# Optimization experiments

Measured on AMD Instinct MI355X. Metric: run time of the kernel, lower is better.

The kernel has to match this reference:

```python
import jax, jax.numpy as jnp
import numpy as np

B, T, NL, H, IN, OUT = 64, 25, 2, 2048, 66, 66
HT_LIMIT = 1.0  # hardtanh clamp


def setup_inputs() -> dict:
    key = jax.random.key(0)
    ks = jax.random.split(key, 14)
    s = 0.02  # small init like uniform(-1/sqrt(H), 1/sqrt(H))
    return {
        "inputs": jax.random.normal(ks[0], (B, IN), jnp.float32),
        "hiddens": jax.random.normal(ks[1], (NL, B, H), jnp.float32) * 0.1,
        "cells": jax.random.normal(ks[2], (NL, B, H), jnp.float32) * 0.1,
        "W_ih0": jax.random.normal(ks[3], (4 * H, IN), jnp.float32) * s,
        "W_hh0": jax.random.normal(ks[4], (4 * H, H), jnp.float32) * s,
        "b_ih0": jax.random.normal(ks[5], (4 * H,), jnp.float32) * s,
        "b_hh0": jax.random.normal(ks[6], (4 * H,), jnp.float32) * s,
        "W_ih1": jax.random.normal(ks[7], (4 * H, H), jnp.float32) * s,
        "W_hh1": jax.random.normal(ks[8], (4 * H, H), jnp.float32) * s,
        "b_ih1": jax.random.normal(ks[9], (4 * H,), jnp.float32) * s,
        "b_hh1": jax.random.normal(ks[10], (4 * H,), jnp.float32) * s,
        "fc_w": jax.random.normal(ks[11], (OUT, H), jnp.float32) * s,
        "fc_b": jax.random.normal(ks[12], (OUT,), jnp.float32) * s,
    }


def _lstm_cell(x, h, c, Wih, Whh, bih, bhh):
    # torch.nn.LSTMCell math: gates ordered i, f, g, o
    g = x @ Wih.T + bih + h @ Whh.T + bhh  # [B, 4H]
    i, f, gg, o = jnp.split(g, 4, axis=-1)
    i = jax.nn.sigmoid(i)
    f = jax.nn.sigmoid(f)
    gg = jnp.tanh(gg)
    o = jax.nn.sigmoid(o)
    c2 = f * c + i * gg
    h2 = o * jnp.tanh(c2)
    return h2, c2


def reference(inputs, hiddens, cells, W_ih0, W_hh0, b_ih0, b_hh0,
              W_ih1, W_hh1, b_ih1, b_hh1, fc_w, fc_b):
    params = [(W_ih0, W_hh0, b_ih0, b_hh0), (W_ih1, W_hh1, b_ih1, b_hh1)]
    # dropout p = 0.0 -> identity on inputs

    def step(carry, _):
        x, hs, cs = carry  # hs, cs: [NL, B, H]
        new_h, new_c = [], []
        layer_in = x
        for l, (Wih, Whh, bih, bhh) in enumerate(params):
            h2, c2 = _lstm_cell(layer_in, hs[l], cs[l], Wih, Whh, bih, bhh)
            new_h.append(h2)
            new_c.append(c2)
            layer_in = h2
        out = jnp.clip(new_h[-1] @ fc_w.T + fc_b, -HT_LIMIT, HT_LIMIT)  # hardtanh
        x_next = jax.lax.stop_gradient(out)  # output.detach() feedback
        return (x_next, jnp.stack(new_h), jnp.stack(new_c)), out

    _, outs = jax.lax.scan(step, (inputs, hiddens, cells), None, length=T)
    return jnp.transpose(outs, (1, 0, 2))  # [B, T, OUT]
```

## Files before the change

kernel.cpp:

```cpp
#include <hip/hip_runtime.h>
#include <hip/hip_bf16.h>


typedef short bfrag  __attribute__((ext_vector_type(8)));
typedef float accv   __attribute__((ext_vector_type(4)));
typedef float vfloat4 __attribute__((ext_vector_type(4)));
typedef unsigned short usvec8 __attribute__((ext_vector_type(8)));

#define LD8(p) (*(const bfrag*)(p))

__device__ __forceinline__ unsigned short f2bf(float x) {
    unsigned int u = __float_as_uint(x);
    unsigned int r = u + 0x7FFFu + ((u >> 16) & 1u);
    return (unsigned short)(r >> 16);
}
__device__ __forceinline__ float bf2f(unsigned short u) {
    return __uint_as_float(((unsigned int)u) << 16);
}

__device__ __forceinline__ int ap_idx(int b, int j, int KC) {
    return (((b >> 4) * KC + (j >> 5)) << 9) + ((((j >> 3) & 3) * 16 + (b & 15)) << 3) + (j & 7);
}


__global__ __launch_bounds__(256) void cast_big(
        const float* __restrict__ s0, const float* __restrict__ s1, const float* __restrict__ s2,
        unsigned short* __restrict__ d0, unsigned short* __restrict__ d1, unsigned short* __restrict__ d2) {
    unsigned int tid = blockIdx.x * 256 + threadIdx.x;
    unsigned int a = tid >> 21;
    unsigned int r = tid & 2097151u;
    const float* src = (a == 0) ? s0 : (a == 1) ? s1 : s2;
    unsigned short* dst = (a == 0) ? d0 : (a == 1) ? d1 : d2;
    unsigned int lane = r & 63u;
    unsigned int kc   = (r >> 6) & 63u;
    unsigned int p    = (r >> 12) & 1u;
    unsigned int jb   = r >> 13;
    unsigned int n = lane & 15u, quad = lane >> 4;
    unsigned int row = (2u * p + (n >> 3)) * 2048u + jb * 8u + (n & 7u);
    unsigned int k0  = kc * 32u + quad * 8u;
    const float* sp = src + (size_t)row * 2048 + k0;
    vfloat4 v0 = *(const vfloat4*)sp;
    vfloat4 v1 = *(const vfloat4*)(sp + 4);
    usvec8 u = { f2bf(v0.x), f2bf(v0.y), f2bf(v0.z), f2bf(v0.w),
                 f2bf(v1.x), f2bf(v1.y), f2bf(v1.z), f2bf(v1.w) };
    *(usvec8*)(dst + (size_t)r * 8) = u;
}

__global__ __launch_bounds__(256) void init_state(
        const float* __restrict__ inputs, const float* __restrict__ hiddens,
        const float* __restrict__ cells,  const float* __restrict__ wih0,
        unsigned short* __restrict__ wih0p,
        unsigned short* __restrict__ h0, unsigned short* __restrict__ h1,
        float* __restrict__ c0, float* __restrict__ c1,
        unsigned short* __restrict__ xb,
        float* __restrict__ bsum0, float* __restrict__ bsum1,
        const float* __restrict__ bih0, const float* __restrict__ bhh0,
        const float* __restrict__ bih1, const float* __restrict__ bhh1) {
    int i = blockIdx.x * 256 + threadIdx.x;
    if (i < 786432) {
        int jo = i & 7, lane = (i >> 3) & 63;
        int t2 = i >> 9, kc = t2 % 3, t3 = t2 / 3, p = t3 & 1, jb = t3 >> 1;
        int n = lane & 15, quad = lane >> 4;
        int row = (2 * p + (n >> 3)) * 2048 + jb * 8 + (n & 7);
        int k = kc * 32 + quad * 8 + jo;
        wih0p[i] = (k < 66) ? f2bf(wih0[row * 66 + k]) : (unsigned short)0;
        return;
    }
    i -= 786432;
    if (i < 131072) { int b = i >> 11, j = i & 2047; h0[ap_idx(b, j, 64)] = f2bf(hiddens[i]); return; }
    i -= 131072;
    if (i < 131072) { int b = i >> 11, j = i & 2047; h1[ap_idx(b, j, 64)] = f2bf(hiddens[131072 + i]); return; }
    i -= 131072;
    if (i < 131072) { int b = i >> 11, j = i & 2047; c0[(j >> 3) * 512 + b * 8 + (j & 7)] = cells[i]; return; }
    i -= 131072;
    if (i < 131072) { int b = i >> 11, j = i & 2047; c1[(j >> 3) * 512 + b * 8 + (j & 7)] = cells[131072 + i]; return; }
    i -= 131072;
    if (i < 16384) {
        int jo = i & 7, lane = (i >> 3) & 63;
        int t2 = i >> 9;
        int kc = t2 & 7, m = t2 >> 3;
        int b = m * 16 + (lane & 15);
        int k = kc * 32 + (lane >> 4) * 8 + jo;
        xb[i] = (k < 66) ? f2bf(inputs[b * 66 + k]) : (unsigned short)0;
        return;
    }
    i -= 16384;
    if (i < 8192) { bsum0[i] = bih0[i] + bhh0[i]; return; }
    i -= 8192;
    if (i < 8192) { bsum1[i] = bih1[i] + bhh1[i]; }
}

template<bool L0>
__global__ __launch_bounds__(512, 4) void lstm3(
        const unsigned short* __restrict__ Ap1, const unsigned short* __restrict__ Bp1,
        const unsigned short* __restrict__ Ap2, const unsigned short* __restrict__ Bp2,
        const float* __restrict__ bsum,
        float* __restrict__ c_state,
        unsigned short* __restrict__ h_out) {
    __shared__ float gsm[8][64][32];
    int tid = threadIdx.x, lane = tid & 63, w = tid >> 6;
    int jb = blockIdx.x;
    constexpr int N1  = L0 ? 1 : 8;
    constexpr int N2  = 8;
    constexpr int NC  = N1 + N2;
    constexpr int KA1 = L0 ? 8 : 64;
    constexpr int KB1 = L0 ? 3 : 64;
    constexpr int KC2 = 64;
    constexpr int PF  = 2;

    int kB1 = L0 ? (w < 3 ? w : 0) : w;
    const unsigned short* a1 = Ap1 + ((size_t)w << 9) + lane * 8;
    const unsigned short* b1 = Bp1 + (((size_t)(2 * jb) * KB1 + kB1) << 9) + lane * 8;
    const unsigned short* a2 = Ap2 + ((size_t)w << 9) + lane * 8;
    const unsigned short* b2 = Bp2 + (((size_t)(2 * jb) * KC2 + w) << 9) + lane * 8;

    accv acc[4][2] = {};
    bfrag fA[PF][4], fB[PF][2];

    auto issue = [&](int i) {
        int s = i % PF;
        const unsigned short *ap, *bp;
        int sa, sb;
        if (i < N1) { ap = a1 + ((size_t)i << 12); bp = b1 + ((size_t)i << 12); sa = KA1 << 9; sb = KB1 << 9; }
        else { int ii = i - N1; ap = a2 + ((size_t)ii << 12); bp = b2 + ((size_t)ii << 12); sa = KC2 << 9; sb = KC2 << 9; }
        fA[s][0] = LD8(ap);
        fA[s][1] = LD8(ap + sa);
        fA[s][2] = LD8(ap + 2 * sa);
        fA[s][3] = LD8(ap + 3 * sa);
        fB[s][0] = LD8(bp);
        fB[s][1] = LD8(bp + sb);
    };

    #pragma unroll
    for (int i = 0; i < PF; ++i) issue(i);
    #pragma unroll
    for (int i = 0; i < NC; ++i) {
        int s = i % PF;
        #pragma unroll
        for (int mi = 0; mi < 4; ++mi)
            #pragma unroll
            for (int p = 0; p < 2; ++p)
                acc[mi][p] = __builtin_amdgcn_mfma_f32_16x16x32_bf16(fA[s][mi], fB[s][p], acc[mi][p], 0, 0, 0);
        if (i + PF < NC) issue(i + PF);
    }

    int n = lane & 15, quad = lane >> 4;
    #pragma unroll
    for (int mi = 0; mi < 4; ++mi)
        #pragma unroll
        for (int p = 0; p < 2; ++p)
            #pragma unroll
            for (int r = 0; r < 4; ++r) {
                int R = mi * 16 + quad * 4 + r;
                int C = p * 16 + n;
                gsm[w][R][C ^ ((R & 3) << 3)] = acc[mi][p][r];
            }
    __syncthreads();

    int b = tid >> 3, jj = tid & 7;
    float g4[4];
    #pragma unroll
    for (int g = 0; g < 4; ++g) {
        int Cp = (g * 8 + jj) ^ ((b & 3) << 3);
        float s = 0.f;
        #pragma unroll
        for (int w8 = 0; w8 < 8; ++w8) s += gsm[w8][b][Cp];
        g4[g] = s;
    }
    int j = jb * 8 + jj;
    float gi = g4[0] + bsum[j];
    float gf = g4[1] + bsum[2048 + j];
    float gg = g4[2] + bsum[4096 + j];
    float go = g4[3] + bsum[6144 + j];
    float iv = 1.f / (1.f + __expf(-gi));
    float fv = 1.f / (1.f + __expf(-gf));
    float gv = tanhf(gg);
    float ov = 1.f / (1.f + __expf(-go));
    float cp = c_state[jb * 512 + tid];
    float cn = fv * cp + iv * gv;
    float hn = ov * tanhf(cn);
    c_state[jb * 512 + tid] = cn;
    h_out[ap_idx(b, j, 64)] = f2bf(hn);
}

__global__ __launch_bounds__(512) void fc2(
        const unsigned short* __restrict__ h1,
        const float* __restrict__ fcw,
        const float* __restrict__ fcb,
        float* __restrict__ out,
        unsigned short* __restrict__ xb,
        int t) {
    __shared__ float red[8][64];
    int o = blockIdx.x;
    int b = threadIdx.x & 63, w = threadIdx.x >> 6;
    const float* wrow = fcw + (size_t)o * 2048;
    float acc = 0.f;
    for (int kc = w; kc < 64; kc += 8) {
        const unsigned short* hp = h1 + (((size_t)(b >> 4) * 64 + kc) << 9) + (b & 15) * 8;
        const float* wp = wrow + kc * 32;
        #pragma unroll
        for (int q = 0; q < 4; ++q) {
            usvec8 hv = *(const usvec8*)(hp + q * 128);
            vfloat4 w0 = *(const vfloat4*)(wp + q * 8);
            vfloat4 w1 = *(const vfloat4*)(wp + q * 8 + 4);
            acc = fmaf(bf2f(hv[0]), w0.x, acc);
            acc = fmaf(bf2f(hv[1]), w0.y, acc);
            acc = fmaf(bf2f(hv[2]), w0.z, acc);
            acc = fmaf(bf2f(hv[3]), w0.w, acc);
            acc = fmaf(bf2f(hv[4]), w1.x, acc);
            acc = fmaf(bf2f(hv[5]), w1.y, acc);
            acc = fmaf(bf2f(hv[6]), w1.z, acc);
            acc = fmaf(bf2f(hv[7]), w1.w, acc);
        }
    }
    red[w][b] = acc;
    __syncthreads();
    if (threadIdx.x < 64) {
        int bb = threadIdx.x;
        float v = fcb[o];
        #pragma unroll
        for (int q = 0; q < 8; ++q) v += red[q][bb];
        v = fminf(1.f, fmaxf(-1.f, v));
        out[((size_t)bb * 25 + t) * 66 + o] = v;
        int kc = o >> 5;
        xb[(((size_t)(bb >> 4) * 8 + kc) << 9) + ((((o >> 3) & 3) * 16 + (bb & 15)) << 3) + (o & 7)] = f2bf(v);
    }
}

extern "C" void kernel_launch(void* const* d_in, const int* in_sizes, int n_in,
                              void* d_out, int out_size, void* d_ws, size_t ws_size,
                              hipStream_t stream) {
    (void)in_sizes; (void)n_in; (void)out_size; (void)ws_size;
    const float* inputs  = (const float*)d_in[0];
    const float* hiddens = (const float*)d_in[1];
    const float* cells   = (const float*)d_in[2];
    const float* W_ih0   = (const float*)d_in[3];
    const float* W_hh0   = (const float*)d_in[4];
    const float* b_ih0   = (const float*)d_in[5];
    const float* b_hh0   = (const float*)d_in[6];
    const float* W_ih1   = (const float*)d_in[7];
    const float* W_hh1   = (const float*)d_in[8];
    const float* b_ih1   = (const float*)d_in[9];
    const float* b_hh1   = (const float*)d_in[10];
    const float* fc_w    = (const float*)d_in[11];
    const float* fc_b    = (const float*)d_in[12];
    float* out = (float*)d_out;

    unsigned short* whh0p = (unsigned short*)d_ws;
    unsigned short* wih1p = whh0p + 16777216;
    unsigned short* whh1p = wih1p + 16777216;
    unsigned short* wih0p = whh1p + 16777216;
    unsigned short* h0a   = wih0p + 786432;
    unsigned short* h0b   = h0a + 131072;
    unsigned short* h1a   = h0b + 131072;
    unsigned short* h1b   = h1a + 131072;
    unsigned short* xb    = h1b + 131072;
    float* c0    = (float*)(xb + 16384);
    float* c1    = c0 + 131072;
    float* bsum0 = c1 + 131072;
    float* bsum1 = bsum0 + 8192;

    cast_big<<<24576, 256, 0, stream>>>(W_hh0, W_ih1, W_hh1, whh0p, wih1p, whh1p);
    init_state<<<5248, 256, 0, stream>>>(inputs, hiddens, cells, W_ih0,
                                         wih0p, h0a, h1a, c0, c1, xb,
                                         bsum0, bsum1, b_ih0, b_hh0, b_ih1, b_hh1);

    unsigned short* h0buf[2] = {h0a, h0b};
    unsigned short* h1buf[2] = {h1a, h1b};
    for (int t = 0; t < 25; ++t) {
        int cur = t & 1, nxt = cur ^ 1;
        lstm3<true><<<256, 512, 0, stream>>>(xb, wih0p,
                                             h0buf[cur], whh0p,
                                             bsum0, c0, h0buf[nxt]);
        lstm3<false><<<256, 512, 0, stream>>>(h0buf[nxt], wih1p,
                                              h1buf[cur], whh1p,
                                              bsum1, c1, h1buf[nxt]);
        fc2<<<66, 512, 0, stream>>>(h1buf[nxt], fc_w, fc_b, out, xb, t);
    }
}
```

Baseline: 978.6 us.

## Fuse FC projection into LSTM layer kernels via atomic partial sums

Removes the separate fc2 kernel each timestep. Layer-1 blocks compute their slice's contribution to the FC output and atomically add it into a per-timestep fp32 workspace. The next step's layer-0 kernel applies bias, clamp and bf16 conversion to build its input in shared memory, and a small finalize kernel handles the last step. The two setup kernels are merged into one, and the prefetch depth rises to 3 while launch bounds drop occupancy to 2. This cuts 25 launches and one serial stage per step, at the cost of many atomics and redundant clamp work in every layer-0 block.

```diff
diff --git a/kernel.cpp b/kernel.cpp
--- a/kernel.cpp
+++ b/kernel.cpp
@@ -14,39 +14,15 @@
     unsigned int r = u + 0x7FFFu + ((u >> 16) & 1u);
     return (unsigned short)(r >> 16);
 }
-__device__ __forceinline__ float bf2f(unsigned short u) {
-    return __uint_as_float(((unsigned int)u) << 16);
-}
 
 __device__ __forceinline__ int ap_idx(int b, int j, int KC) {
     return (((b >> 4) * KC + (j >> 5)) << 9) + ((((j >> 3) & 3) * 16 + (b & 15)) << 3) + (j & 7);
 }
 
 
-__global__ __launch_bounds__(256) void cast_big(
+__global__ __launch_bounds__(256) void prep(
         const float* __restrict__ s0, const float* __restrict__ s1, const float* __restrict__ s2,
-        unsigned short* __restrict__ d0, unsigned short* __restrict__ d1, unsigned short* __restrict__ d2) {
-    unsigned int tid = blockIdx.x * 256 + threadIdx.x;
-    unsigned int a = tid >> 21;
-    unsigned int r = tid & 2097151u;
-    const float* src = (a == 0) ? s0 : (a == 1) ? s1 : s2;
-    unsigned short* dst = (a == 0) ? d0 : (a == 1) ? d1 : d2;
-    unsigned int lane = r & 63u;
-    unsigned int kc   = (r >> 6) & 63u;
-    unsigned int p    = (r >> 12) & 1u;
-    unsigned int jb   = r >> 13;
-    unsigned int n = lane & 15u, quad = lane >> 4;
-    unsigned int row = (2u * p + (n >> 3)) * 2048u + jb * 8u + (n & 7u);
-    unsigned int k0  = kc * 32u + quad * 8u;
-    const float* sp = src + (size_t)row * 2048 + k0;
-    vfloat4 v0 = *(const vfloat4*)sp;
-    vfloat4 v1 = *(const vfloat4*)(sp + 4);
-    usvec8 u = { f2bf(v0.x), f2bf(v0.y), f2bf(v0.z), f2bf(v0.w),
-                 f2bf(v1.x), f2bf(v1.y), f2bf(v1.z), f2bf(v1.w) };
-    *(usvec8*)(dst + (size_t)r * 8) = u;
-}
-
-__global__ __launch_bounds__(256) void init_state(
+        unsigned short* __restrict__ d0, unsigned short* __restrict__ d1, unsigned short* __restrict__ d2,
         const float* __restrict__ inputs, const float* __restrict__ hiddens,
         const float* __restrict__ cells,  const float* __restrict__ wih0,
         unsigned short* __restrict__ wih0p,
@@ -55,8 +31,31 @@
         unsigned short* __restrict__ xb,
         float* __restrict__ bsum0, float* __restrict__ bsum1,
         const float* __restrict__ bih0, const float* __restrict__ bhh0,
-        const float* __restrict__ bih1, const float* __restrict__ bhh1) {
-    int i = blockIdx.x * 256 + threadIdx.x;
+        const float* __restrict__ bih1, const float* __restrict__ bhh1,
+        float* __restrict__ ows) {
+    int bid = blockIdx.x;
+    if (bid < 24576) {
+        unsigned int tid = bid * 256 + threadIdx.x;
+        unsigned int a = tid >> 21;
+        unsigned int r = tid & 2097151u;
+        const float* src = (a == 0) ? s0 : (a == 1) ? s1 : s2;
+        unsigned short* dst = (a == 0) ? d0 : (a == 1) ? d1 : d2;
+        unsigned int lane = r & 63u;
+        unsigned int kc   = (r >> 6) & 63u;
+        unsigned int p    = (r >> 12) & 1u;
+        unsigned int jb   = r >> 13;
+        unsigned int n = lane & 15u, quad = lane >> 4;
+        unsigned int row = (2u * p + (n >> 3)) * 2048u + jb * 8u + (n & 7u);
+        unsigned int k0  = kc * 32u + quad * 8u;
+        const float* sp = src + (size_t)row * 2048 + k0;
+        vfloat4 v0 = *(const vfloat4*)sp;
+        vfloat4 v1 = *(const vfloat4*)(sp + 4);
+        usvec8 u = { f2bf(v0.x), f2bf(v0.y), f2bf(v0.z), f2bf(v0.w),
+                     f2bf(v1.x), f2bf(v1.y), f2bf(v1.z), f2bf(v1.w) };
+        *(usvec8*)(dst + (size_t)r * 8) = u;
+        return;
+    }
+    int i = (bid - 24576) * 256 + threadIdx.x;
     if (i < 786432) {
         int jo = i & 7, lane = (i >> 3) & 63;
         int t2 = i >> 9, kc = t2 % 3, t3 = t2 / 3, p = t3 & 1, jb = t3 >> 1;
@@ -75,62 +74,169 @@
     i -= 131072;
     if (i < 131072) { int b = i >> 11, j = i & 2047; c1[(j >> 3) * 512 + b * 8 + (j & 7)] = cells[131072 + i]; return; }
     i -= 131072;
-    if (i < 16384) {
+    if (i < 6144) {
         int jo = i & 7, lane = (i >> 3) & 63;
-        int t2 = i >> 9;
-        int kc = t2 & 7, m = t2 >> 3;
+        int t2 = i >> 9, kc = t2 % 3, m = t2 / 3;
         int b = m * 16 + (lane & 15);
         int k = kc * 32 + (lane >> 4) * 8 + jo;
         xb[i] = (k < 66) ? f2bf(inputs[b * 66 + k]) : (unsigned short)0;
         return;
     }
-    i -= 16384;
+    i -= 6144;
     if (i < 8192) { bsum0[i] = bih0[i] + bhh0[i]; return; }
     i -= 8192;
-    if (i < 8192) { bsum1[i] = bih1[i] + bhh1[i]; }
-}
-
-template<bool L0>
-__global__ __launch_bounds__(512, 4) void lstm3(
-        const unsigned short* __restrict__ Ap1, const unsigned short* __restrict__ Bp1,
-        const unsigned short* __restrict__ Ap2, const unsigned short* __restrict__ Bp2,
+    if (i < 8192) { bsum1[i] = bih1[i] + bhh1[i]; return; }
+    i -= 8192;
+    if (i < 105600) { ows[i] = 0.f; }
+}
+
+__global__ __launch_bounds__(512, 2) void lstm_l0(
+        const unsigned short* __restrict__ xb,
+        const unsigned short* __restrict__ Bp1,
+        const unsigned short* __restrict__ Ap2,
+        const unsigned short* __restrict__ Bp2,
         const float* __restrict__ bsum,
+        const float* __restrict__ ows,
+        const float* __restrict__ fcb,
+        float* __restrict__ outg, int tprev,
         float* __restrict__ c_state,
         unsigned short* __restrict__ h_out) {
     __shared__ float gsm[8][64][32];
+    __shared__ unsigned short xsm[64][104];
     int tid = threadIdx.x, lane = tid & 63, w = tid >> 6;
     int jb = blockIdx.x;
-    constexpr int N1  = L0 ? 1 : 8;
-    constexpr int N2  = 8;
-    constexpr int NC  = N1 + N2;
-    constexpr int KA1 = L0 ? 8 : 64;
-    constexpr int KB1 = L0 ? 3 : 64;
-    constexpr int KC2 = 64;
-    constexpr int PF  = 2;
-
-    int kB1 = L0 ? (w < 3 ? w : 0) : w;
+
+    if (ows) {
+        for (int i = tid; i < (64 * 104) / 2; i += 512) ((unsigned int*)xsm)[i] = 0u;
+        __syncthreads();
+        for (int idx = tid; idx < 4224; idx += 512) {
+            int o = idx >> 6, b = idx & 63;
+            float v = ows[idx] + fcb[o];
+            v = fminf(1.f, fmaxf(-1.f, v));
+            if (jb == 0) outg[((size_t)b * 25 + tprev) * 66 + o] = v;
+            xsm[b][o] = f2bf(v);
+        }
+        __syncthreads();
+    }
+
+    constexpr int PF = 3, NC = 8;
+    accv acc[4][2] = {};
+
+    bfrag xa[4], xw[2];
+    bool s1 = (w < 3);
+    if (s1) {
+        const unsigned short* bp = Bp1 + (((size_t)(2 * jb) * 3 + w) << 9) + lane * 8;
+        xw[0] = LD8(bp);
+        xw[1] = LD8(bp + (3 << 9));
+        if (ows) {
+            int n15 = lane & 15, k0 = w * 32 + (lane >> 4) * 8;
+            #pragma unroll
+            for (int mi = 0; mi < 4; ++mi) xa[mi] = *(const bfrag*)&xsm[mi * 16 + n15][k0];
+        } else {
+            #pragma unroll
+            for (int mi = 0; mi < 4; ++mi) xa[mi] = LD8(xb + (((size_t)mi * 3 + w) << 9) + lane * 8);
+        }
+    }
+
+    const unsigned short* a2 = Ap2 + ((size_t)w << 9) + lane * 8;
+    const unsigned short* b2 = Bp2 + (((size_t)(2 * jb) * 64 + w) << 9) + lane * 8;
+    bfrag fA[PF][4], fB[PF][2];
+    auto issue = [&](int i) {
+        int s = i % PF;
+        const unsigned short* ap = a2 + ((size_t)i << 12);
+        const unsigned short* bp = b2 + ((size_t)i << 12);
+        fA[s][0] = LD8(ap);
+        fA[s][1] = LD8(ap + (64 << 9));
+        fA[s][2] = LD8(ap + 2 * (64 << 9));
+        fA[s][3] = LD8(ap + 3 * (64 << 9));
+        fB[s][0] = LD8(bp);
+        fB[s][1] = LD8(bp + (64 << 9));
+    };
+    #pragma unroll
+    for (int i = 0; i < PF; ++i) issue(i);
+    if (s1) {
+        #pragma unroll
+        for (int mi = 0; mi < 4; ++mi)
+            #pragma unroll
+            for (int p = 0; p < 2; ++p)
+                acc[mi][p] = __builtin_amdgcn_mfma_f32_16x16x32_bf16(xa[mi], xw[p], acc[mi][p], 0, 0, 0);
+    }
+    #pragma unroll
+    for (int i = 0; i < NC; ++i) {
+        int s = i % PF;
+        #pragma unroll
+        for (int mi = 0; mi < 4; ++mi)
+            #pragma unroll
+            for (int p = 0; p < 2; ++p)
+                acc[mi][p] = __builtin_amdgcn_mfma_f32_16x16x32_bf16(fA[s][mi], fB[s][p], acc[mi][p], 0, 0, 0);
+        if (i + PF < NC) issue(i + PF);
+    }
+
+    int n15 = lane & 15, quad = lane >> 4;
+    #pragma unroll
+    for (int mi = 0; mi < 4; ++mi)
+        #pragma unroll
+        for (int p = 0; p < 2; ++p)
+            #pragma unroll
+            for (int r = 0; r < 4; ++r) {
+                int R = mi * 16 + quad * 4 + r;
+                int C = p * 16 + n15;
+                gsm[w][R][C ^ ((R & 3) << 3)] = acc[mi][p][r];
+            }
+    __syncthreads();
+    int b = tid >> 3, jj = tid & 7;
+    float g4[4];
+    #pragma unroll
+    for (int g = 0; g < 4; ++g) {
+        int Cp = (g * 8 + jj) ^ ((b & 3) << 3);
+        float s = 0.f;
+        #pragma unroll
+        for (int w8 = 0; w8 < 8; ++w8) s += gsm[w8][b][Cp];
+        g4[g] = s;
+    }
+    int j = jb * 8 + jj;
+    float iv = 1.f / (1.f + __expf(-(g4[0] + bsum[j])));
+    float fv = 1.f / (1.f + __expf(-(g4[1] + bsum[2048 + j])));
+    float gv = tanhf(g4[2] + bsum[4096 + j]);
+    float ov = 1.f / (1.f + __expf(-(g4[3] + bsum[6144 + j])));
+    float cn = fv * c_state[jb * 512 + tid] + iv * gv;
+    float hn = ov * tanhf(cn);
+    c_state[jb * 512 + tid] = cn;
+    h_out[ap_idx(b, j, 64)] = f2bf(hn);
+}
+
+__global__ __launch_bounds__(512, 2) void lstm_l1(
+        const unsigned short* __restrict__ Ap1,
+        const unsigned short* __restrict__ Bp1,
+        const unsigned short* __restrict__ Ap2,
+        const unsigned short* __restrict__ Bp2,
+        const float* __restrict__ bsum,
+        float* __restrict__ c_state,
+        unsigned short* __restrict__ h_out,
+        const float* __restrict__ fcw,
+        float* __restrict__ ows_t) {
+    __shared__ float gsm[8][64][32];
+    int tid = threadIdx.x, lane = tid & 63, w = tid >> 6;
+    int jb = blockIdx.x;
+    constexpr int PF = 3, NC = 16;
     const unsigned short* a1 = Ap1 + ((size_t)w << 9) + lane * 8;
-    const unsigned short* b1 = Bp1 + (((size_t)(2 * jb) * KB1 + kB1) << 9) + lane * 8;
+    const unsigned short* b1 = Bp1 + (((size_t)(2 * jb) * 64 + w) << 9) + lane * 8;
     const unsigned short* a2 = Ap2 + ((size_t)w << 9) + lane * 8;
-    const unsigned short* b2 = Bp2 + (((size_t)(2 * jb) * KC2 + w) << 9) + lane * 8;
-
+    const unsigned short* b2 = Bp2 + (((size_t)(2 * jb) * 64 + w) << 9) + lane * 8;
     accv acc[4][2] = {};
     bfrag fA[PF][4], fB[PF][2];
-
     auto issue = [&](int i) {
         int s = i % PF;
         const unsigned short *ap, *bp;
-        int sa, sb;
-        if (i < N1) { ap = a1 + ((size_t)i << 12); bp = b1 + ((size_t)i << 12); sa = KA1 << 9; sb = KB1 << 9; }
-        else { int ii = i - N1; ap = a2 + ((size_t)ii << 12); bp = b2 + ((size_t)ii << 12); sa = KC2 << 9; sb = KC2 << 9; }
+        if (i < 8) { ap = a1 + ((size_t)i << 12); bp = b1 + ((size_t)i << 12); }
+        else       { ap = a2 + ((size_t)(i - 8) << 12); bp = b2 + ((size_t)(i - 8) << 12); }
         fA[s][0] = LD8(ap);
-        fA[s][1] = LD8(ap + sa);
-        fA[s][2] = LD8(ap + 2 * sa);
-        fA[s][3] = LD8(ap + 3 * sa);
+        fA[s][1] = LD8(ap + (64 << 9));
+        fA[s][2] = LD8(ap + 2 * (64 << 9));
+        fA[s][3] = LD8(ap + 3 * (64 << 9));
         fB[s][0] = LD8(bp);
-        fB[s][1] = LD8(bp + sb);
+        fB[s][1] = LD8(bp + (64 << 9));
     };
-
     #pragma unroll
     for (int i = 0; i < PF; ++i) issue(i);
     #pragma unroll
@@ -144,7 +250,7 @@
         if (i + PF < NC) issue(i + PF);
     }
 
-    int n = lane & 15, quad = lane >> 4;
+    int n15 = lane & 15, quad = lane >> 4;
     #pragma unroll
     for (int mi = 0; mi < 4; ++mi)
         #pragma unroll
@@ -152,11 +258,10 @@
             #pragma unroll
             for (int r = 0; r < 4; ++r) {
                 int R = mi * 16 + quad * 4 + r;
-                int C = p * 16 + n;
+                int C = p * 16 + n15;
                 gsm[w][R][C ^ ((R & 3) << 3)] = acc[mi][p][r];
             }
     __syncthreads();
-
     int b = tid >> 3, jj = tid & 7;
     float g4[4];
     #pragma unroll
@@ -168,62 +273,38 @@
         g4[g] = s;
     }
     int j = jb * 8 + jj;
-    float gi = g4[0] + bsum[j];
-    float gf = g4[1] + bsum[2048 + j];
-    float gg = g4[2] + bsum[4096 + j];
-    float go = g4[3] + bsum[6144 + j];
-    float iv = 1.f / (1.f + __expf(-gi));
-    float fv = 1.f / (1.f + __expf(-gf));
-    float gv = tanhf(gg);
-    float ov = 1.f / (1.f + __expf(-go));
-    float cp = c_state[jb * 512 + tid];
-    float cn = fv * cp + iv * gv;
+    float iv = 1.f / (1.f + __expf(-(g4[0] + bsum[j])));
+    float fv = 1.f / (1.f + __expf(-(g4[1] + bsum[2048 + j])));
+    float gv = tanhf(g4[2] + bsum[4096 + j]);
+    float ov = 1.f / (1.f + __expf(-(g4[3] + bsum[6144 + j])));
+    float cn = fv * c_state[jb * 512 + tid] + iv * gv;
     float hn = ov * tanhf(cn);
     c_state[jb * 512 + tid] = cn;
     h_out[ap_idx(b, j, 64)] = f2bf(hn);
-}
-
-__global__ __launch_bounds__(512) void fc2(
-        const unsigned short* __restrict__ h1,
-        const float* __restrict__ fcw,
-        const float* __restrict__ fcb,
-        float* __restrict__ out,
-        unsigned short* __restrict__ xb,
-        int t) {
-    __shared__ float red[8][64];
-    int o = blockIdx.x;
-    int b = threadIdx.x & 63, w = threadIdx.x >> 6;
-    const float* wrow = fcw + (size_t)o * 2048;
-    float acc = 0.f;
-    for (int kc = w; kc < 64; kc += 8) {
-        const unsigned short* hp = h1 + (((size_t)(b >> 4) * 64 + kc) << 9) + (b & 15) * 8;
-        const float* wp = wrow + kc * 32;
-        #pragma unroll
-        for (int q = 0; q < 4; ++q) {
-            usvec8 hv = *(const usvec8*)(hp + q * 128);
-            vfloat4 w0 = *(const vfloat4*)(wp + q * 8);
-            vfloat4 w1 = *(const vfloat4*)(wp + q * 8 + 4);
-            acc = fmaf(bf2f(hv[0]), w0.x, acc);
-            acc = fmaf(bf2f(hv[1]), w0.y, acc);
-            acc = fmaf(bf2f(hv[2]), w0.z, acc);
-            acc = fmaf(bf2f(hv[3]), w0.w, acc);
-            acc = fmaf(bf2f(hv[4]), w1.x, acc);
-            acc = fmaf(bf2f(hv[5]), w1.y, acc);
-            acc = fmaf(bf2f(hv[6]), w1.z, acc);
-            acc = fmaf(bf2f(hv[7]), w1.w, acc);
-        }
-    }
-    red[w][b] = acc;
+
     __syncthreads();
-    if (threadIdx.x < 64) {
-        int bb = threadIdx.x;
-        float v = fcb[o];
-        #pragma unroll
-        for (int q = 0; q < 8; ++q) v += red[q][bb];
+    float* hs = &gsm[0][0][0];
+    hs[b * 9 + jj] = hn;
+    __syncthreads();
+    for (int idx = tid; idx < 4224; idx += 512) {
+        int o = idx >> 6, b2 = idx & 63;
+        const float* wc = fcw + (size_t)o * 2048 + jb * 8;
+        float s = 0.f;
+        #pragma unroll
+        for (int q = 0; q < 8; ++q) s = fmaf(hs[b2 * 9 + q], wc[q], s);
+        atomicAdd(ows_t + idx, s);
+    }
+}
+
+__global__ __launch_bounds__(256) void finalize(
+        const float* __restrict__ ows24, const float* __restrict__ fcb,
+        float* __restrict__ outg) {
+    int idx = blockIdx.x * 256 + threadIdx.x;
+    if (idx < 4224) {
+        int o = idx >> 6, b = idx & 63;
+        float v = ows24[idx] + fcb[o];
         v = fminf(1.f, fmaxf(-1.f, v));
-        out[((size_t)bb * 25 + t) * 66 + o] = v;
-        int kc = o >> 5;
-        xb[(((size_t)(bb >> 4) * 8 + kc) << 9) + ((((o >> 3) & 3) * 16 + (bb & 15)) << 3) + (o & 7)] = f2bf(v);
+        outg[((size_t)b * 25 + 24) * 66 + o] = v;
     }
 }
 
@@ -255,26 +336,26 @@
     unsigned short* h1a   = h0b + 131072;
     unsigned short* h1b   = h1a + 131072;
     unsigned short* xb    = h1b + 131072;
-    float* c0    = (float*)(xb + 16384);
+    float* c0    = (float*)(xb + 6144);
     float* c1    = c0 + 131072;
     float* bsum0 = c1 + 131072;
     float* bsum1 = bsum0 + 8192;
-
-    cast_big<<<24576, 256, 0, stream>>>(W_hh0, W_ih1, W_hh1, whh0p, wih1p, whh1p);
-    init_state<<<5248, 256, 0, stream>>>(inputs, hiddens, cells, W_ih0,
-                                         wih0p, h0a, h1a, c0, c1, xb,
-                                         bsum0, bsum1, b_ih0, b_hh0, b_ih1, b_hh1);
+    float* ows   = bsum1 + 8192;
+
+    prep<<<30198, 256, 0, stream>>>(W_hh0, W_ih1, W_hh1, whh0p, wih1p, whh1p,
+                                    inputs, hiddens, cells, W_ih0,
+                                    wih0p, h0a, h1a, c0, c1, xb,
+                                    bsum0, bsum1, b_ih0, b_hh0, b_ih1, b_hh1, ows);
 
     unsigned short* h0buf[2] = {h0a, h0b};
     unsigned short* h1buf[2] = {h1a, h1b};
     for (int t = 0; t < 25; ++t) {
         int cur = t & 1, nxt = cur ^ 1;
-        lstm3<true><<<256, 512, 0, stream>>>(xb, wih0p,
-                                             h0buf[cur], whh0p,
-                                             bsum0, c0, h0buf[nxt]);
-        lstm3<false><<<256, 512, 0, stream>>>(h0buf[nxt], wih1p,
-                                              h1buf[cur], whh1p,
-                                              bsum1, c1, h1buf[nxt]);
-        fc2<<<66, 512, 0, stream>>>(h1buf[nxt], fc_w, fc_b, out, xb, t);
-    }
-}
+        lstm_l0<<<256, 512, 0, stream>>>(xb, wih0p, h0buf[cur], whh0p, bsum0,
+                                         t == 0 ? (const float*)nullptr : ows + (t - 1) * 4224,
+                                         fc_b, out, t - 1, c0, h0buf[nxt]);
+        lstm_l1<<<256, 512, 0, stream>>>(h0buf[nxt], wih1p, h1buf[cur], whh1p, bsum1,
+                                         c1, h1buf[nxt], fc_w, ows + t * 4224);
+    }
+    finalize<<<17, 256, 0, stream>>>(ows + 24 * 4224, fc_b, out);
+}
```

Measured after the change: 1.130 ms. +15.5%, slower.

## Split recurrent GEMMs off the critical path and overlap them with FC

Applied to the files above, without the earlier changes.

Restructures each timestep. One kernel now computes both layers' hidden-to-hidden GEMMs (W_hh0·h0, W_hh1·h1) in parallel with the previous step's FC head, writing partial gates to global memory. Two lighter cell kernels then finish with the small input GEMMs plus the nonlinearities. The two prep kernels are merged into one launch, the padded x buffer shrinks to three k-chunks, and h double-buffering is dropped because the recurrent GEMMs read h before the cell kernels overwrite it. The serial chain per step becomes more parallel at the cost of extra global traffic for the partial gates.

```diff
diff --git a/kernel.cpp b/kernel.cpp
--- a/kernel.cpp
+++ b/kernel.cpp
@@ -23,30 +23,9 @@
 }
 
 
-__global__ __launch_bounds__(256) void cast_big(
+__global__ __launch_bounds__(256) void prep(
         const float* __restrict__ s0, const float* __restrict__ s1, const float* __restrict__ s2,
-        unsigned short* __restrict__ d0, unsigned short* __restrict__ d1, unsigned short* __restrict__ d2) {
-    unsigned int tid = blockIdx.x * 256 + threadIdx.x;
-    unsigned int a = tid >> 21;
-    unsigned int r = tid & 2097151u;
-    const float* src = (a == 0) ? s0 : (a == 1) ? s1 : s2;
-    unsigned short* dst = (a == 0) ? d0 : (a == 1) ? d1 : d2;
-    unsigned int lane = r & 63u;
-    unsigned int kc   = (r >> 6) & 63u;
-    unsigned int p    = (r >> 12) & 1u;
-    unsigned int jb   = r >> 13;
-    unsigned int n = lane & 15u, quad = lane >> 4;
-    unsigned int row = (2u * p + (n >> 3)) * 2048u + jb * 8u + (n & 7u);
-    unsigned int k0  = kc * 32u + quad * 8u;
-    const float* sp = src + (size_t)row * 2048 + k0;
-    vfloat4 v0 = *(const vfloat4*)sp;
-    vfloat4 v1 = *(const vfloat4*)(sp + 4);
-    usvec8 u = { f2bf(v0.x), f2bf(v0.y), f2bf(v0.z), f2bf(v0.w),
-                 f2bf(v1.x), f2bf(v1.y), f2bf(v1.z), f2bf(v1.w) };
-    *(usvec8*)(dst + (size_t)r * 8) = u;
-}
-
-__global__ __launch_bounds__(256) void init_state(
+        unsigned short* __restrict__ d0, unsigned short* __restrict__ d1, unsigned short* __restrict__ d2,
         const float* __restrict__ inputs, const float* __restrict__ hiddens,
         const float* __restrict__ cells,  const float* __restrict__ wih0,
         unsigned short* __restrict__ wih0p,
@@ -56,7 +35,29 @@
         float* __restrict__ bsum0, float* __restrict__ bsum1,
         const float* __restrict__ bih0, const float* __restrict__ bhh0,
         const float* __restrict__ bih1, const float* __restrict__ bhh1) {
-    int i = blockIdx.x * 256 + threadIdx.x;
+    int bid = blockIdx.x;
+    if (bid < 24576) {
+        unsigned int tid = bid * 256 + threadIdx.x;
+        unsigned int a = tid >> 21;
+        unsigned int r = tid & 2097151u;
+        const float* src = (a == 0) ? s0 : (a == 1) ? s1 : s2;
+        unsigned short* dst = (a == 0) ? d0 : (a == 1) ? d1 : d2;
+        unsigned int lane = r & 63u;
+        unsigned int kc   = (r >> 6) & 63u;
+        unsigned int p    = (r >> 12) & 1u;
+        unsigned int jb   = r >> 13;
+        unsigned int n = lane & 15u, quad = lane >> 4;
+        unsigned int row = (2u * p + (n >> 3)) * 2048u + jb * 8u + (n & 7u);
+        unsigned int k0  = kc * 32u + quad * 8u;
+        const float* sp = src + (size_t)row * 2048 + k0;
+        vfloat4 v0 = *(const vfloat4*)sp;
+        vfloat4 v1 = *(const vfloat4*)(sp + 4);
+        usvec8 u = { f2bf(v0.x), f2bf(v0.y), f2bf(v0.z), f2bf(v0.w),
+                     f2bf(v1.x), f2bf(v1.y), f2bf(v1.z), f2bf(v1.w) };
+        *(usvec8*)(dst + (size_t)r * 8) = u;
+        return;
+    }
+    int i = (bid - 24576) * 256 + threadIdx.x;
     if (i < 786432) {
         int jo = i & 7, lane = (i >> 3) & 63;
         int t2 = i >> 9, kc = t2 % 3, t3 = t2 / 3, p = t3 & 1, jb = t3 >> 1;
@@ -75,62 +76,38 @@
     i -= 131072;
     if (i < 131072) { int b = i >> 11, j = i & 2047; c1[(j >> 3) * 512 + b * 8 + (j & 7)] = cells[131072 + i]; return; }
     i -= 131072;
-    if (i < 16384) {
+    if (i < 6144) {
         int jo = i & 7, lane = (i >> 3) & 63;
-        int t2 = i >> 9;
-        int kc = t2 & 7, m = t2 >> 3;
+        int t2 = i >> 9, kc = t2 % 3, m = t2 / 3;
         int b = m * 16 + (lane & 15);
         int k = kc * 32 + (lane >> 4) * 8 + jo;
         xb[i] = (k < 66) ? f2bf(inputs[b * 66 + k]) : (unsigned short)0;
         return;
     }
-    i -= 16384;
+    i -= 6144;
     if (i < 8192) { bsum0[i] = bih0[i] + bhh0[i]; return; }
     i -= 8192;
     if (i < 8192) { bsum1[i] = bih1[i] + bhh1[i]; }
 }
 
-template<bool L0>
-__global__ __launch_bounds__(512, 4) void lstm3(
-        const unsigned short* __restrict__ Ap1, const unsigned short* __restrict__ Bp1,
-        const unsigned short* __restrict__ Ap2, const unsigned short* __restrict__ Bp2,
-        const float* __restrict__ bsum,
-        float* __restrict__ c_state,
-        unsigned short* __restrict__ h_out) {
-    __shared__ float gsm[8][64][32];
-    int tid = threadIdx.x, lane = tid & 63, w = tid >> 6;
-    int jb = blockIdx.x;
-    constexpr int N1  = L0 ? 1 : 8;
-    constexpr int N2  = 8;
-    constexpr int NC  = N1 + N2;
-    constexpr int KA1 = L0 ? 8 : 64;
-    constexpr int KB1 = L0 ? 3 : 64;
-    constexpr int KC2 = 64;
-    constexpr int PF  = 2;
-
-    int kB1 = L0 ? (w < 3 ? w : 0) : w;
-    const unsigned short* a1 = Ap1 + ((size_t)w << 9) + lane * 8;
-    const unsigned short* b1 = Bp1 + (((size_t)(2 * jb) * KB1 + kB1) << 9) + lane * 8;
-    const unsigned short* a2 = Ap2 + ((size_t)w << 9) + lane * 8;
-    const unsigned short* b2 = Bp2 + (((size_t)(2 * jb) * KC2 + w) << 9) + lane * 8;
-
-    accv acc[4][2] = {};
+__device__ __forceinline__ void gemm8(const unsigned short* __restrict__ Ap,
+                                      const unsigned short* __restrict__ Bp,
+                                      int jb, int lane, int w, accv (&acc)[4][2]) {
+    constexpr int PF = 2, NC = 8;
+    const unsigned short* a = Ap + ((size_t)w << 9) + lane * 8;
+    const unsigned short* b = Bp + (((size_t)(2 * jb) * 64 + w) << 9) + lane * 8;
     bfrag fA[PF][4], fB[PF][2];
-
     auto issue = [&](int i) {
         int s = i % PF;
-        const unsigned short *ap, *bp;
-        int sa, sb;
-        if (i < N1) { ap = a1 + ((size_t)i << 12); bp = b1 + ((size_t)i << 12); sa = KA1 << 9; sb = KB1 << 9; }
-        else { int ii = i - N1; ap = a2 + ((size_t)ii << 12); bp = b2 + ((size_t)ii << 12); sa = KC2 << 9; sb = KC2 << 9; }
+        const unsigned short* ap = a + ((size_t)i << 12);
+        const unsigned short* bp = b + ((size_t)i << 12);
         fA[s][0] = LD8(ap);
-        fA[s][1] = LD8(ap + sa);
-        fA[s][2] = LD8(ap + 2 * sa);
-        fA[s][3] = LD8(ap + 3 * sa);
+        fA[s][1] = LD8(ap + (64 << 9));
+        fA[s][2] = LD8(ap + 2 * (64 << 9));
+        fA[s][3] = LD8(ap + 3 * (64 << 9));
         fB[s][0] = LD8(bp);
-        fB[s][1] = LD8(bp + sb);
+        fB[s][1] = LD8(bp + (64 << 9));
     };
-
     #pragma unroll
     for (int i = 0; i < PF; ++i) issue(i);
     #pragma unroll
@@ -143,7 +120,10 @@
                 acc[mi][p] = __builtin_amdgcn_mfma_f32_16x16x32_bf16(fA[s][mi], fB[s][p], acc[mi][p], 0, 0, 0);
         if (i + PF < NC) issue(i + PF);
     }
-
+}
+
+__device__ __forceinline__ void store_gsm(float (*gsm)[64][32], accv (&acc)[4][2],
+                                          int lane, int w) {
     int n = lane & 15, quad = lane >> 4;
     #pragma unroll
     for (int mi = 0; mi < 4; ++mi)
@@ -155,76 +135,149 @@
                 int C = p * 16 + n;
                 gsm[w][R][C ^ ((R & 3) << 3)] = acc[mi][p][r];
             }
+}
+
+__global__ __launch_bounds__(512, 4) void pstep(
+        const unsigned short* __restrict__ h0, const unsigned short* __restrict__ h1,
+        const unsigned short* __restrict__ Bp0, const unsigned short* __restrict__ Bp1,
+        const float* __restrict__ fcw, const float* __restrict__ fcb,
+        float* __restrict__ gp0, float* __restrict__ gp1,
+        unsigned short* __restrict__ xbuf,
+        float* __restrict__ outg, int t) {
+    __shared__ float gsm[8][64][32];
+    int tid = threadIdx.x, lane = tid & 63, w = tid >> 6;
+    int bid = blockIdx.x;
+
+    if (bid < 66) {
+        if (t == 0) return;
+        int o = bid, b = lane;
+        const float* wrow = fcw + (size_t)o * 2048;
+        float acc = 0.f;
+        for (int kc = w; kc < 64; kc += 8) {
+            const unsigned short* hp = h1 + (((size_t)(b >> 4) * 64 + kc) << 9) + (b & 15) * 8;
+            const float* wp = wrow + kc * 32;
+            #pragma unroll
+            for (int q = 0; q < 4; ++q) {
+                usvec8 hv = *(const usvec8*)(hp + q * 128);
+                vfloat4 w0 = *(const vfloat4*)(wp + q * 8);
+                vfloat4 w1 = *(const vfloat4*)(wp + q * 8 + 4);
+                acc = fmaf(bf2f(hv[0]), w0.x, acc);
+                acc = fmaf(bf2f(hv[1]), w0.y, acc);
+                acc = fmaf(bf2f(hv[2]), w0.z, acc);
+                acc = fmaf(bf2f(hv[3]), w0.w, acc);
+                acc = fmaf(bf2f(hv[4]), w1.x, acc);
+                acc = fmaf(bf2f(hv[5]), w1.y, acc);
+                acc = fmaf(bf2f(hv[6]), w1.z, acc);
+                acc = fmaf(bf2f(hv[7]), w1.w, acc);
+            }
+        }
+        float* red = &gsm[0][0][0];
+        red[w * 64 + b] = acc;
+        __syncthreads();
+        if (tid < 64) {
+            int bb = tid;
+            float v = fcb[o];
+            #pragma unroll
+            for (int q = 0; q < 8; ++q) v += red[q * 64 + bb];
+            v = fminf(1.f, fmaxf(-1.f, v));
+            outg[((size_t)bb * 25 + (t - 1)) * 66 + o] = v;
+            xbuf[ap_idx(bb, o, 3)] = f2bf(v);
+        }
+        return;
+    }
+
+    int l  = (bid - 66) >> 8;
+    int jb = (bid - 66) & 255;
+    const unsigned short* Ap = l ? h1 : h0;
+    const unsigned short* Bp = l ? Bp1 : Bp0;
+    float* gp = l ? gp1 : gp0;
+    accv acc[4][2] = {};
+    gemm8(Ap, Bp, jb, lane, w, acc);
+    store_gsm(gsm, acc, lane, w);
     __syncthreads();
-
+    for (int idx = tid; idx < 2048; idx += 512) {
+        int b = idx >> 5, C = idx & 31;
+        int Cs = C ^ ((b & 3) << 3);
+        float s = 0.f;
+        #pragma unroll
+        for (int w8 = 0; w8 < 8; ++w8) s += gsm[w8][b][Cs];
+        gp[(size_t)jb * 2048 + idx] = s;
+    }
+}
+
+__global__ __launch_bounds__(512, 4) void c0step(
+        const unsigned short* __restrict__ xbuf, const unsigned short* __restrict__ Bp,
+        const float* __restrict__ gp0, const float* __restrict__ bsum,
+        float* __restrict__ c_state, unsigned short* __restrict__ h_out) {
+    __shared__ float gsm[8][64][32];
+    int tid = threadIdx.x, lane = tid & 63, w = tid >> 6;
+    int jb = blockIdx.x;
+    accv acc[4][2] = {};
+    if (w < 3) {
+        const unsigned short* bp = Bp + (((size_t)(2 * jb) * 3 + w) << 9) + lane * 8;
+        bfrag xw0 = LD8(bp), xw1 = LD8(bp + (3 << 9));
+        #pragma unroll
+        for (int mi = 0; mi < 4; ++mi) {
+            bfrag xa = LD8(xbuf + (((size_t)mi * 3 + w) << 9) + lane * 8);
+            acc[mi][0] = __builtin_amdgcn_mfma_f32_16x16x32_bf16(xa, xw0, acc[mi][0], 0, 0, 0);
+            acc[mi][1] = __builtin_amdgcn_mfma_f32_16x16x32_bf16(xa, xw1, acc[mi][1], 0, 0, 0);
+        }
+    }
+    store_gsm(gsm, acc, lane, w);
+    __syncthreads();
     int b = tid >> 3, jj = tid & 7;
+    const float* gpt = gp0 + (size_t)jb * 2048 + b * 32 + jj;
     float g4[4];
     #pragma unroll
     for (int g = 0; g < 4; ++g) {
         int Cp = (g * 8 + jj) ^ ((b & 3) << 3);
-        float s = 0.f;
+        float s = gpt[g * 8];
         #pragma unroll
         for (int w8 = 0; w8 < 8; ++w8) s += gsm[w8][b][Cp];
         g4[g] = s;
     }
     int j = jb * 8 + jj;
-    float gi = g4[0] + bsum[j];
-    float gf = g4[1] + bsum[2048 + j];
-    float gg = g4[2] + bsum[4096 + j];
-    float go = g4[3] + bsum[6144 + j];
-    float iv = 1.f / (1.f + __expf(-gi));
-    float fv = 1.f / (1.f + __expf(-gf));
-    float gv = tanhf(gg);
-    float ov = 1.f / (1.f + __expf(-go));
-    float cp = c_state[jb * 512 + tid];
-    float cn = fv * cp + iv * gv;
+    float iv = 1.f / (1.f + __expf(-(g4[0] + bsum[j])));
+    float fv = 1.f / (1.f + __expf(-(g4[1] + bsum[2048 + j])));
+    float gv = tanhf(g4[2] + bsum[4096 + j]);
+    float ov = 1.f / (1.f + __expf(-(g4[3] + bsum[6144 + j])));
+    float cn = fv * c_state[jb * 512 + tid] + iv * gv;
     float hn = ov * tanhf(cn);
     c_state[jb * 512 + tid] = cn;
     h_out[ap_idx(b, j, 64)] = f2bf(hn);
 }
 
-__global__ __launch_bounds__(512) void fc2(
-        const unsigned short* __restrict__ h1,
-        const float* __restrict__ fcw,
-        const float* __restrict__ fcb,
-        float* __restrict__ out,
-        unsigned short* __restrict__ xb,
-        int t) {
-    __shared__ float red[8][64];
-    int o = blockIdx.x;
-    int b = threadIdx.x & 63, w = threadIdx.x >> 6;
-    const float* wrow = fcw + (size_t)o * 2048;
-    float acc = 0.f;
-    for (int kc = w; kc < 64; kc += 8) {
-        const unsigned short* hp = h1 + (((size_t)(b >> 4) * 64 + kc) << 9) + (b & 15) * 8;
-        const float* wp = wrow + kc * 32;
-        #pragma unroll
-        for (int q = 0; q < 4; ++q) {
-            usvec8 hv = *(const usvec8*)(hp + q * 128);
-            vfloat4 w0 = *(const vfloat4*)(wp + q * 8);
-            vfloat4 w1 = *(const vfloat4*)(wp + q * 8 + 4);
-            acc = fmaf(bf2f(hv[0]), w0.x, acc);
-            acc = fmaf(bf2f(hv[1]), w0.y, acc);
-            acc = fmaf(bf2f(hv[2]), w0.z, acc);
-            acc = fmaf(bf2f(hv[3]), w0.w, acc);
-            acc = fmaf(bf2f(hv[4]), w1.x, acc);
-            acc = fmaf(bf2f(hv[5]), w1.y, acc);
-            acc = fmaf(bf2f(hv[6]), w1.z, acc);
-            acc = fmaf(bf2f(hv[7]), w1.w, acc);
-        }
-    }
-    red[w][b] = acc;
+__global__ __launch_bounds__(512, 4) void c1step(
+        const unsigned short* __restrict__ h0new, const unsigned short* __restrict__ Bp,
+        const float* __restrict__ gp1, const float* __restrict__ bsum,
+        float* __restrict__ c_state, unsigned short* __restrict__ h_out) {
+    __shared__ float gsm[8][64][32];
+    int tid = threadIdx.x, lane = tid & 63, w = tid >> 6;
+    int jb = blockIdx.x;
+    accv acc[4][2] = {};
+    gemm8(h0new, Bp, jb, lane, w, acc);
+    store_gsm(gsm, acc, lane, w);
     __syncthreads();
-    if (threadIdx.x < 64) {
-        int bb = threadIdx.x;
-        float v = fcb[o];
-        #pragma unroll
-        for (int q = 0; q < 8; ++q) v += red[q][bb];
-        v = fminf(1.f, fmaxf(-1.f, v));
-        out[((size_t)bb * 25 + t) * 66 + o] = v;
-        int kc = o >> 5;
-        xb[(((size_t)(bb >> 4) * 8 + kc) << 9) + ((((o >> 3) & 3) * 16 + (bb & 15)) << 3) + (o & 7)] = f2bf(v);
-    }
+    int b = tid >> 3, jj = tid & 7;
+    const float* gpt = gp1 + (size_t)jb * 2048 + b * 32 + jj;
+    float g4[4];
+    #pragma unroll
+    for (int g = 0; g < 4; ++g) {
+        int Cp = (g * 8 + jj) ^ ((b & 3) << 3);
+        float s = gpt[g * 8];
+        #pragma unroll
+        for (int w8 = 0; w8 < 8; ++w8) s += gsm[w8][b][Cp];
+        g4[g] = s;
+    }
+    int j = jb * 8 + jj;
+    float iv = 1.f / (1.f + __expf(-(g4[0] + bsum[j])));
+    float fv = 1.f / (1.f + __expf(-(g4[1] + bsum[2048 + j])));
+    float gv = tanhf(g4[2] + bsum[4096 + j]);
+    float ov = 1.f / (1.f + __expf(-(g4[3] + bsum[6144 + j])));
+    float cn = fv * c_state[jb * 512 + tid] + iv * gv;
+    float hn = ov * tanhf(cn);
+    c_state[jb * 512 + tid] = cn;
+    h_out[ap_idx(b, j, 64)] = f2bf(hn);
 }
 
 extern "C" void kernel_launch(void* const* d_in, const int* in_sizes, int n_in,
@@ -250,31 +303,27 @@
     unsigned short* wih1p = whh0p + 16777216;
     unsigned short* whh1p = wih1p + 16777216;
     unsigned short* wih0p = whh1p + 16777216;
-    unsigned short* h0a   = wih0p + 786432;
-    unsigned short* h0b   = h0a + 131072;
-    unsigned short* h1a   = h0b + 131072;
-    unsigned short* h1b   = h1a + 131072;
-    unsigned short* xb    = h1b + 131072;
-    float* c0    = (float*)(xb + 16384);
+    unsigned short* h0    = wih0p + 786432;
+    unsigned short* h1    = h0 + 131072;
+    unsigned short* xb    = h1 + 131072;
+    float* c0    = (float*)(xb + 6144);
     float* c1    = c0 + 131072;
     float* bsum0 = c1 + 131072;
     float* bsum1 = bsum0 + 8192;
-
-    cast_big<<<24576, 256, 0, stream>>>(W_hh0, W_ih1, W_hh1, whh0p, wih1p, whh1p);
-    init_state<<<5248, 256, 0, stream>>>(inputs, hiddens, cells, W_ih0,
-                                         wih0p, h0a, h1a, c0, c1, xb,
-                                         bsum0, bsum1, b_ih0, b_hh0, b_ih1, b_hh1);
-
-    unsigned short* h0buf[2] = {h0a, h0b};
-    unsigned short* h1buf[2] = {h1a, h1b};
+    float* gp0   = bsum1 + 8192;
+    float* gp1   = gp0 + 524288;
+
+    prep<<<29784, 256, 0, stream>>>(W_hh0, W_ih1, W_hh1, whh0p, wih1p, whh1p,
+                                    inputs, hiddens, cells, W_ih0,
+                                    wih0p, h0, h1, c0, c1, xb,
+                                    bsum0, bsum1, b_ih0, b_hh0, b_ih1, b_hh1);
+
     for (int t = 0; t < 25; ++t) {
-        int cur = t & 1, nxt = cur ^ 1;
-        lstm3<true><<<256, 512, 0, stream>>>(xb, wih0p,
-                                             h0buf[cur], whh0p,
-                                             bsum0, c0, h0buf[nxt]);
-        lstm3<false><<<256, 512, 0, stream>>>(h0buf[nxt], wih1p,
-                                              h1buf[cur], whh1p,
-                                              bsum1, c1, h1buf[nxt]);
-        fc2<<<66, 512, 0, stream>>>(h1buf[nxt], fc_w, fc_b, out, xb, t);
-    }
-}
+        pstep<<<578, 512, 0, stream>>>(h0, h1, whh0p, whh1p, fc_w, fc_b,
+                                       gp0, gp1, xb, out, t);
+        c0step<<<256, 512, 0, stream>>>(xb, wih0p, gp0, bsum0, c0, h0);
+        c1step<<<256, 512, 0, stream>>>(h0, wih1p, gp1, bsum1, c1, h1);
+    }
+    pstep<<<66, 512, 0, stream>>>(h0, h1, whh0p, whh1p, fc_w, fc_b,
+                                  gp0, gp1, xb, out, 25);
+}
```

After: 953.1 us. 1.03x faster.
